# Performance work log

Measured on AMD Instinct MI355X. Metric: run time of the kernel, lower is better.

Reference implementation:

```python
import jax, jax.numpy as jnp
import numpy as np

NUM_HEADS = 16
NEG_INF = -1e9  # matches torch source's -1000000000.0 additive mask
ROPE_BASE = 10000.0


def _rope(t):
    """Rotary position embedding, half-rotation form. t: [B, H, S, D]."""
    D = t.shape[-1]
    S = t.shape[2]
    inv_freq = 1.0 / (ROPE_BASE ** (jnp.arange(0, D, 2, dtype=jnp.float32) / D))  # [D/2]
    pos = jnp.arange(S, dtype=jnp.float32)
    freqs = pos[:, None] * inv_freq[None, :]          # [S, D/2]
    cos = jnp.cos(freqs)[None, None]                  # [1,1,S,D/2]
    sin = jnp.sin(freqs)[None, None]
    t1, t2 = t[..., : D // 2], t[..., D // 2 :]
    return jnp.concatenate([t1 * cos - t2 * sin, t1 * sin + t2 * cos], axis=-1)


def setup_inputs() -> dict:
    key = jax.random.key(0)
    kx, kq, kk, kv, ko = jax.random.split(key, 5)
    B, S, Dm = 2, 2048, 1024
    w_scale = 0.02
    return {
        "x": jax.random.normal(kx, (B, S, Dm), dtype=jnp.float32),
        "attention_mask": jnp.ones((B, S), dtype=jnp.float32),
        "Wq": jax.random.normal(kq, (Dm, Dm), dtype=jnp.float32) * w_scale,
        "Wk": jax.random.normal(kk, (Dm, Dm), dtype=jnp.float32) * w_scale,
        "Wv": jax.random.normal(kv, (Dm, Dm), dtype=jnp.float32) * w_scale,
        "Wo": jax.random.normal(ko, (Dm, Dm), dtype=jnp.float32) * w_scale,
    }


def reference(x, attention_mask, Wq, Wk, Wv, Wo):
    B, S, Dm = x.shape
    H = NUM_HEADS
    Hd = Dm // H

    def to_heads(t):  # [B,S,Dm] -> [B,H,S,Hd]
        return t.reshape(B, S, H, Hd).transpose(0, 2, 1, 3)

    q = _rope(to_heads(x @ Wq))
    k = _rope(to_heads(x @ Wk))
    v = to_heads(x @ Wv)

    scaling = 1.0 / np.sqrt(Hd).astype(np.float32)
    scores = jnp.einsum("bhqd,bhkd->bhqk", q, k) * scaling  # [B,H,S,S]

    # causal additive mask (triu of -1e9 above diagonal), as in apply_masking
    causal = jnp.triu(jnp.full((S, S), NEG_INF, dtype=scores.dtype), k=1)
    # padding mask: (1 - mask) * -1e9 broadcast to [B,1,1,S]
    amask = (1.0 - attention_mask)[:, None, None, :] * NEG_INF
    scores = scores + causal[None, None] + amask

    weights = jax.nn.softmax(scores, axis=-1)
    out = jnp.einsum("bhqk,bhkd->bhqd", weights, v)  # [B,H,S,Hd]
    out = out.transpose(0, 2, 1, 3).reshape(B, S, Dm)
    return out @ Wo
```

## Files before the change

### kernel.cpp

```cpp
#include <hip/hip_runtime.h>

typedef unsigned short u16;
typedef unsigned int u32;
typedef __attribute__((ext_vector_type(8))) short short8;
typedef __attribute__((ext_vector_type(4))) short s4v;
typedef __attribute__((ext_vector_type(4))) float f32x4;

#define S_LEN 2048
#define NH 16
#define HD 64
#define DM 1024

#if __has_builtin(__builtin_amdgcn_mfma_f32_16x16x16_bf16)
#define MFMA_K16(a, b, c) __builtin_amdgcn_mfma_f32_16x16x16_bf16(a, b, c, 0, 0, 0)
#else
#define MFMA_K16(a, b, c) __builtin_amdgcn_mfma_f32_16x16x16bf16_1k(a, b, c, 0, 0, 0)
#endif

__device__ __forceinline__ u16 f2bf(float f) {
    union { float f; u32 u; } v; v.f = f;
    u32 u = v.u;
    u32 r = u + 0x7fffu + ((u >> 16) & 1u);
    return (u16)(r >> 16);
}
__device__ __forceinline__ float bf2f(u16 h) {
    union { u32 u; float f; } v; v.u = ((u32)h) << 16;
    return v.f;
}

__device__ __forceinline__ u32 cvtpk_bf16(float lo, float hi) {
    u32 r;
    asm("v_cvt_pk_bf16_f32 %0, %1, %2" : "=v"(r) : "v"(lo), "v"(hi));
    return r;
}

__device__ __forceinline__ void load_lds16(const u16* g, u16* l) {
    __builtin_amdgcn_global_load_lds((const __attribute__((address_space(1))) void*)g,
                                     (__attribute__((address_space(3))) void*)l, 16, 0, 0);
}

__global__ __launch_bounds__(256) void cvt_bf16(const float* __restrict__ in, u16* __restrict__ out, int n) {
    int i = (blockIdx.x * 256 + threadIdx.x) * 4;
    if (i < n) {
        float4 v = *(const float4*)(in + i);
        ushort4 o;
        o.x = f2bf(v.x); o.y = f2bf(v.y); o.z = f2bf(v.z); o.w = f2bf(v.w);
        *(ushort4*)(out + i) = o;
    }
}

__global__ __launch_bounds__(256) void transpose_w4(const float* __restrict__ W0, const float* __restrict__ W1,
                                                    const float* __restrict__ W2, const float* __restrict__ W3,
                                                    u16* __restrict__ T0, u16* __restrict__ T1,
                                                    u16* __restrict__ T2, u16* __restrict__ T3) {
    __shared__ float tile[32][33];
    int z = blockIdx.z;
    const float* W = (z == 0) ? W0 : (z == 1) ? W1 : (z == 2) ? W2 : W3;
    u16* Wt = (z == 0) ? T0 : (z == 1) ? T1 : (z == 2) ? T2 : T3;
    int tx = threadIdx.x, ty = threadIdx.y;
    int k0 = blockIdx.y * 32, n0 = blockIdx.x * 32;
    #pragma unroll
    for (int j = 0; j < 32; j += 8)
        tile[ty + j][tx] = W[(size_t)(k0 + ty + j) * DM + n0 + tx];
    __syncthreads();
    #pragma unroll
    for (int j = 0; j < 32; j += 8)
        Wt[(size_t)(n0 + ty + j) * DM + k0 + tx] = f2bf(tile[tx][ty + j]);
}

template<int MODE, int NI>
__global__ __launch_bounds__(256) void gemm128(const u16* __restrict__ A, const u16* __restrict__ Bt,
                                               u16* __restrict__ Qh, u16* __restrict__ Kh,
                                               u16* __restrict__ Vh, float* __restrict__ Cf) {
    __shared__ u16 Al[128 * 64];
    __shared__ u16 Bl[NI * 32 * 64];
    const int K = DM;
    int tid = threadIdx.x;
    int wave = tid >> 6, lane = tid & 63, g = lane >> 4, ln = lane & 15;
    int wm = (wave >> 1) * 64, wn = (wave & 1) * (NI * 16);
    size_t mb0 = (size_t)blockIdx.y * 128, nb0 = (size_t)blockIdx.x * (NI * 32);

    f32x4 acc[4][NI];
    #pragma unroll
    for (int i = 0; i < 4; i++)
        #pragma unroll
        for (int j = 0; j < NI; j++)
            acc[i][j] = (f32x4){0.f, 0.f, 0.f, 0.f};

    int srow = lane >> 3;
    int scol = (lane & 7) ^ srow;
    const u16* Ag = A + (mb0 + wave * 32 + srow) * K + scol * 8;
    u16* Alw = Al + wave * 2048;
    const u16* Bg;
    u16* Blw;
    if (NI == 4) {
        Bg = Bt + (nb0 + wave * 32 + srow) * K + scol * 8;
        Blw = Bl + wave * 2048;
    } else {
        Bg = Bt + (nb0 + wave * 16 + srow) * K + scol * 8;
        Blw = Bl + wave * 1024;
    }
    int cswz = ln & 7;

    #pragma unroll
    for (int c = 0; c < 4; c++)
        load_lds16(Ag + (size_t)(c * 8) * K, Alw + c * 512);
    #pragma unroll
    for (int c = 0; c < (NI == 4 ? 4 : 2); c++)
        load_lds16(Bg + (size_t)(c * 8) * K, Blw + c * 512);

    for (int k0 = 0; k0 < K; k0 += 64) {
        __syncthreads();

        short8 af[2][4], bf[2][NI];
        #pragma unroll
        for (int ks = 0; ks < 2; ks++) {
            #pragma unroll
            for (int i = 0; i < 4; i++)
                af[ks][i] = *(const short8*)&Al[(wm + i * 16 + ln) * 64 + (((ks * 4 + g) ^ cswz) * 8)];
            #pragma unroll
            for (int i = 0; i < NI; i++)
                bf[ks][i] = *(const short8*)&Bl[(wn + i * 16 + ln) * 64 + (((ks * 4 + g) ^ cswz) * 8)];
        }

        __syncthreads();

        if (k0 + 64 < K) {
            #pragma unroll
            for (int c = 0; c < 4; c++)
                load_lds16(Ag + (size_t)(c * 8) * K + k0 + 64, Alw + c * 512);
            #pragma unroll
            for (int c = 0; c < (NI == 4 ? 4 : 2); c++)
                load_lds16(Bg + (size_t)(c * 8) * K + k0 + 64, Blw + c * 512);
        }

        #pragma unroll
        for (int ks = 0; ks < 2; ks++)
            #pragma unroll
            for (int mi = 0; mi < 4; mi++)
                #pragma unroll
                for (int ni = 0; ni < NI; ni++)
                    acc[mi][ni] = __builtin_amdgcn_mfma_f32_16x16x32_bf16(af[ks][mi], bf[ks][ni], acc[mi][ni], 0, 0, 0);
    }

    if (MODE == 1) {
        #pragma unroll
        for (int mi = 0; mi < 4; mi++)
            #pragma unroll
            for (int ni = 0; ni < NI; ni++)
                #pragma unroll
                for (int r = 0; r < 4; r++) {
                    int m = (int)mb0 + wm + mi * 16 + g * 4 + r;
                    int n = (int)nb0 + wn + ni * 16 + ln;
                    Cf[(size_t)m * DM + n] = acc[mi][ni][r];
                }
    } else {
        int nbase = (int)nb0 + wn;
        int which = nbase >> 10;
        int h = (nbase & (DM - 1)) >> 6;
        if (which < 2) {
            u16* dst = (which == 0) ? Qh : Kh;
            float inv0 = exp2f(-0.4152408746976557f * (float)ln);
            float inv1 = exp2f(-0.4152408746976557f * (float)(16 + ln));
            #pragma unroll
            for (int mi = 0; mi < 4; mi++) {
                #pragma unroll
                for (int r = 0; r < 4; r++) {
                    int m = (int)mb0 + wm + mi * 16 + g * 4 + r;
                    int b = m >> 11, s = m & (S_LEN - 1);
                    float fs = (float)s;
                    float sn0, cs0, sn1, cs1;
                    __sincosf(fs * inv0, &sn0, &cs0);
                    __sincosf(fs * inv1, &sn1, &cs1);
                    float a0 = acc[mi][0][r], a1 = acc[mi][1][r];
                    float a2 = acc[mi][2][r], a3 = acc[mi][3][r];
                    size_t base = ((size_t)(b * NH + h) * S_LEN + s) * HD;
                    dst[base + ln]      = f2bf(a0 * cs0 - a2 * sn0);
                    dst[base + 16 + ln] = f2bf(a1 * cs1 - a3 * sn1);
                    dst[base + 32 + ln] = f2bf(a0 * sn0 + a2 * cs0);
                    dst[base + 48 + ln] = f2bf(a1 * sn1 + a3 * cs1);
                }
            }
        } else {
            #pragma unroll
            for (int mi = 0; mi < 4; mi++) {
                #pragma unroll
                for (int r = 0; r < 4; r++) {
                    int m = (int)mb0 + wm + mi * 16 + g * 4 + r;
                    int b = m >> 11, s = m & (S_LEN - 1);
                    size_t base = ((size_t)(b * NH + h) * S_LEN + s) * HD;
                    #pragma unroll
                    for (int ni = 0; ni < 4; ni++)
                        Vh[base + ni * 16 + ln] = f2bf(acc[mi][ni][r]);
                }
            }
        }
    }
}

__global__ __launch_bounds__(256) void vtrans(const u16* __restrict__ Vh, u16* __restrict__ Vt) {
    __shared__ u16 t[64][70];
    int tid = threadIdx.x;
    int s0 = blockIdx.x * 64, bh = blockIdx.y;
    int r = tid >> 2, c = (tid & 3) * 8;
    const u16* src = Vh + ((size_t)bh * S_LEN + s0) * HD;
    *(short8*)&t[r][c]      = *(const short8*)(src + (size_t)r * HD + c);
    *(short8*)&t[r][c + 32] = *(const short8*)(src + (size_t)r * HD + c + 32);
    __syncthreads();
    u16* dst = Vt + ((size_t)bh * HD + r) * S_LEN + s0;
    short8 o0, o1;
    #pragma unroll
    for (int j = 0; j < 8; j++) {
        o0[j] = (short)t[c + j][r];
        o1[j] = (short)t[c + 32 + j][r];
    }
    *(short8*)(dst + c)      = o0;
    *(short8*)(dst + c + 32) = o1;
}

__global__ __launch_bounds__(512, 4) void flash_kernel(const u16* __restrict__ Qh, const u16* __restrict__ Kh,
                                                       const u16* __restrict__ Vt, const float* __restrict__ amask,
                                                       u16* __restrict__ Op0, u16* __restrict__ Op1,
                                                       u16* __restrict__ Op2, u16* __restrict__ Op3,
                                                       float* __restrict__ L0, float* __restrict__ L1,
                                                       float* __restrict__ L2, float* __restrict__ L3) {
    __shared__ u16 Kl[2][64 * 64];
    __shared__ u16 Vl[2][64 * 64];
    __shared__ float Ml[2][64];
    int tid = threadIdx.x;
    int wave = tid >> 6, lane = tid & 63, g = lane >> 4, ln = lane & 15;
    int i = (int)blockIdx.x;
    int xcd = i & 7;
    int j = i >> 3;
    int bh = xcd * 4 + (j >> 6);
    int inner = j & 63;
    int qblk = 15 - (inner >> 2);
    int sp = inner & 3;
    int b = bh >> 4;
    int q0 = qblk * 128 + wave * 16;
    int qv = q0 + ln;
    const u16* Qb = Qh + (size_t)bh * (S_LEN * HD);
    const u16* Kb = Kh + (size_t)bh * (S_LEN * HD);
    const u16* Vb = Vt + (size_t)bh * (S_LEN * HD);
    const float* am = amask + b * S_LEN;

    short8 qa0 = *(const short8*)(Qb + (size_t)(q0 + ln) * HD + g * 8);
    short8 qa1 = *(const short8*)(Qb + (size_t)(q0 + ln) * HD + 32 + g * 8);

    f32x4 O[4];
    #pragma unroll
    for (int i2 = 0; i2 < 4; i2++) O[i2] = (f32x4){0.f, 0.f, 0.f, 0.f};
    f32x4 Osum = (f32x4){0.f, 0.f, 0.f, 0.f};
    const s4v ones = (s4v){(short)0x3F80, (short)0x3F80, (short)0x3F80, (short)0x3F80};
    const float SCL = 0.125f * 1.4426950408889634f;
    const float MSCL = -1.4426950408889634e9f;

    int T = 2 * qblk + 2;
    int srow = tid >> 3, scid = tid & 7, s7 = srow & 7;
    int stoff = srow * 64 + ((scid ^ s7) * 8);
    const u16* KgL = Kb + (size_t)srow * HD + ((scid ^ s7) * 8);
    const u16* VgP = Vb + (size_t)srow * S_LEN + scid * 8;
    bool vswap = (wave & 1);

    int l7 = ln & 7;
    int kc0 = (g ^ l7) * 8;
    int kc1 = ((4 + g) ^ l7) * 8;
    int rbq = ln * 64;
    int vcoff[4];
    #pragma unroll
    for (int n0 = 0; n0 < 4; n0++)
        vcoff[n0] = (((n0 * 2 + (g >> 1)) ^ l7) * 8) + ((((g & 1) ^ (ln >> 3)) & 1) * 4);

    load_lds16(KgL + (size_t)(sp * 64) * HD, &Kl[0][wave * 512]);
    short8 vR = *(const short8*)(VgP + sp * 64);
    float mR = 0.f;
    if (tid < 64) mR = (1.0f - am[sp * 64 + tid]) * MSCL;
    int cur = 0;

    for (int kt = sp; kt < T; kt += 4) {
        int kbase = kt * 64;
        short8 vS = vR;
        if (vswap) vS = __builtin_shufflevector(vR, vR, 4, 5, 6, 7, 0, 1, 2, 3);
        *(short8*)(Vl[cur] + stoff) = vS;
        if (tid < 64) Ml[cur][tid] = mR;
        __syncthreads();

        if (kt + 4 < T) {
            load_lds16(KgL + (size_t)(kbase + 256) * HD, &Kl[cur ^ 1][wave * 512]);
            vR = *(const short8*)(VgP + (kbase + 256));
            if (tid < 64) mR = (1.0f - am[kbase + 256 + tid]) * MSCL;
        }

        if (kbase <= q0 + 15) {
            const u16* Klc = Kl[cur];
            const u16* Vlc = Vl[cur];
            u32 pk[4][2];
            bool needmask = (kbase + 63 > q0);

            if (!needmask) {
                #pragma unroll
                for (int n0 = 0; n0 < 4; n0++) {
                    const u16* kr = Klc + (n0 * 16) * 64 + rbq;
                    short8 kb0 = *(const short8*)(kr + kc0);
                    short8 kb1 = *(const short8*)(kr + kc1);
                    f32x4 sv = (f32x4){0.f, 0.f, 0.f, 0.f};
                    sv = __builtin_amdgcn_mfma_f32_16x16x32_bf16(kb0, qa0, sv, 0, 0, 0);
                    sv = __builtin_amdgcn_mfma_f32_16x16x32_bf16(kb1, qa1, sv, 0, 0, 0);
                    f32x4 mkv = *(f32x4*)&Ml[cur][n0 * 16 + g * 4];
                    float p[4];
                    #pragma unroll
                    for (int r = 0; r < 4; r++)
                        p[r] = exp2f(sv[r] * SCL + mkv[r]);
                    pk[n0][0] = cvtpk_bf16(p[0], p[1]);
                    pk[n0][1] = cvtpk_bf16(p[2], p[3]);
                }
            } else {
                #pragma unroll
                for (int n0 = 0; n0 < 4; n0++) {
                    const u16* kr = Klc + (n0 * 16) * 64 + rbq;
                    short8 kb0 = *(const short8*)(kr + kc0);
                    short8 kb1 = *(const short8*)(kr + kc1);
                    f32x4 sv = (f32x4){0.f, 0.f, 0.f, 0.f};
                    sv = __builtin_amdgcn_mfma_f32_16x16x32_bf16(kb0, qa0, sv, 0, 0, 0);
                    sv = __builtin_amdgcn_mfma_f32_16x16x32_bf16(kb1, qa1, sv, 0, 0, 0);
                    f32x4 mkv = *(f32x4*)&Ml[cur][n0 * 16 + g * 4];
                    int keyb = kbase + n0 * 16 + g * 4;
                    float p[4];
                    #pragma unroll
                    for (int r = 0; r < 4; r++) {
                        float s2 = sv[r] * SCL + mkv[r];
                        if (keyb + r > qv) s2 = -1.0e9f;
                        p[r] = exp2f(s2);
                    }
                    pk[n0][0] = cvtpk_bf16(p[0], p[1]);
                    pk[n0][1] = cvtpk_bf16(p[2], p[3]);
                }
            }

            __builtin_amdgcn_s_setprio(1);
            #pragma unroll
            for (int n0 = 0; n0 < 4; n0++) {
                union { u32 u[2]; s4v v; } pb;
                pb.u[0] = pk[n0][0];
                pb.u[1] = pk[n0][1];
                Osum = MFMA_K16(ones, pb.v, Osum);
            }
            #pragma unroll
            for (int t = 0; t < 4; t++) {
                const u16* vr = Vlc + (t * 16) * 64 + rbq;
                #pragma unroll
                for (int n0 = 0; n0 < 4; n0++) {
                    s4v va = *(const s4v*)(vr + vcoff[n0]);
                    union { u32 u[2]; s4v v; } pb;
                    pb.u[0] = pk[n0][0];
                    pb.u[1] = pk[n0][1];
                    O[t] = MFMA_K16(va, pb.v, O[t]);
                }
            }
            __builtin_amdgcn_s_setprio(0);
        }
        cur ^= 1;
    }

    u16* Od = (sp == 0) ? Op0 : (sp == 1) ? Op1 : (sp == 2) ? Op2 : Op3;
    float* Ld = (sp == 0) ? L0 : (sp == 1) ? L1 : (sp == 2) ? L2 : L3;
    if (lane < 16) Ld[(size_t)bh * S_LEN + q0 + ln] = Osum[0];
    size_t obase = (size_t)bh * (HD * S_LEN) + q0 + ln;
    #pragma unroll
    for (int t = 0; t < 4; t++)
        #pragma unroll
        for (int r = 0; r < 4; r++)
            Od[obase + (size_t)(t * 16 + g * 4 + r) * S_LEN] = f2bf(O[t][r]);
}

__global__ __launch_bounds__(256) void flash_reduce(const u16* __restrict__ Op0, const u16* __restrict__ Op1,
                                                    const u16* __restrict__ Op2, const u16* __restrict__ Op3,
                                                    const float* __restrict__ L0, const float* __restrict__ L1,
                                                    const float* __restrict__ L2, const float* __restrict__ L3,
                                                    u16* __restrict__ attn) {
    __shared__ float t[64][65];
    int tid = threadIdx.x;
    int qt = blockIdx.x, bh = blockIdx.y;
    int b = bh >> 4, h = bh & (NH - 1);
    #pragma unroll
    for (int it = 0; it < 2; it++) {
        int idx = tid + it * 256;
        int d = idx >> 3, c = (idx & 7) * 8;
        size_t off = (size_t)bh * (HD * S_LEN) + (size_t)d * S_LEN + qt * 64 + c;
        short8 a0 = *(const short8*)(Op0 + off);
        short8 a1 = *(const short8*)(Op1 + off);
        short8 a2 = *(const short8*)(Op2 + off);
        short8 a3 = *(const short8*)(Op3 + off);
        #pragma unroll
        for (int j = 0; j < 8; j++)
            t[d][c + j] = bf2f((u16)a0[j]) + bf2f((u16)a1[j]) + bf2f((u16)a2[j]) + bf2f((u16)a3[j]);
    }
    __syncthreads();
    int qr = tid >> 2, dc = (tid & 3) * 16;
    int qg = qt * 64 + qr;
    size_t li = (size_t)bh * S_LEN + qg;
    float inv = 1.0f / (L0[li] + L1[li] + L2[li] + L3[li]);
    short8 o0, o1;
    #pragma unroll
    for (int j = 0; j < 8; j++) {
        o0[j] = (short)f2bf(t[dc + j][qr] * inv);
        o1[j] = (short)f2bf(t[dc + 8 + j][qr] * inv);
    }
    u16* dst = attn + ((size_t)b * S_LEN + qg) * DM + h * HD + dc;
    *(short8*)dst = o0;
    *(short8*)(dst + 8) = o1;
}

extern "C" void kernel_launch(void* const* d_in, const int* in_sizes, int n_in,
                              void* d_out, int out_size, void* d_ws, size_t ws_size,
                              hipStream_t stream) {
    const float* x     = (const float*)d_in[0];
    const float* amask = (const float*)d_in[1];
    const float* Wq    = (const float*)d_in[2];
    const float* Wk    = (const float*)d_in[3];
    const float* Wv    = (const float*)d_in[4];
    const float* Wo    = (const float*)d_in[5];
    float* out = (float*)d_out;
    char* ws = (char*)d_ws;

    u16* x_bf   = (u16*)(ws);
    u16* Op1    = (u16*)(ws);
    u16* Wqkv_t = (u16*)(ws + 8388608);
    float* L0   = (float*)(ws + 8388608);
    float* L1   = (float*)(ws + 8650752);
    float* L2   = (float*)(ws + 8912896);
    float* L3   = (float*)(ws + 9175040);
    u16* Wo_t   = (u16*)(ws + 14680064);
    u16* Qh     = (u16*)(ws + 16777216);
    u16* Kh     = (u16*)(ws + 25165824);
    u16* Vt     = (u16*)(ws + 33554432);
    u16* attnF  = (u16*)(ws + 33554432);
    u16* Vh     = (u16*)(ws + 41943040);
    u16* Op0    = (u16*)(ws + 41943040);
    u16* Op2    = (u16*)d_out;
    u16* Op3    = (u16*)d_out + 4194304;

    cvt_bf16<<<4096, 256, 0, stream>>>(x, x_bf, 2 * S_LEN * DM);

    transpose_w4<<<dim3(32, 32, 4), dim3(32, 8), 0, stream>>>(
        Wq, Wk, Wv, Wo, Wqkv_t, Wqkv_t + 1048576, Wqkv_t + 2097152, Wo_t);

    gemm128<0, 4><<<dim3(24, 32), 256, 0, stream>>>(x_bf, Wqkv_t, Qh, Kh, Vh, nullptr);

    vtrans<<<dim3(32, 2 * NH), 256, 0, stream>>>(Vh, Vt);

    flash_kernel<<<dim3(2048), 512, 0, stream>>>(Qh, Kh, Vt, amask,
                                                 Op0, Op1, Op2, Op3, L0, L1, L2, L3);

    flash_reduce<<<dim3(32, 2 * NH), 256, 0, stream>>>(Op0, Op1, Op2, Op3,
                                                       L0, L1, L2, L3, attnF);

    gemm128<1, 2><<<dim3(16, 32), 256, 0, stream>>>(attnF, Wo_t, nullptr, nullptr, nullptr, out);
}
```

Measured before the change: 189.7 us.

## Halve flash split-K factor to two and fuse prep conversion kernels

The x-to-bf16 conversion and the four weight transposes now run in one launch, which saves a kernel launch. The flash attention split over the key dimension drops from four partitions to two, so the grid shrinks to 1024 blocks and each block loops over twice as many key tiles. The reduce kernel reads only two partial outputs and two partial sums, which cuts memory traffic and removes the use of the output buffer as scratch. The cost is lower parallelism in the flash kernel and a longer serial loop per block, which could hurt occupancy or load balance under causal masking.

```diff
diff --git a/kernel.cpp b/kernel.cpp
--- a/kernel.cpp
+++ b/kernel.cpp
@@ -39,33 +39,36 @@
                                      (__attribute__((address_space(3))) void*)l, 16, 0, 0);
 }
 
-__global__ __launch_bounds__(256) void cvt_bf16(const float* __restrict__ in, u16* __restrict__ out, int n) {
-    int i = (blockIdx.x * 256 + threadIdx.x) * 4;
-    if (i < n) {
-        float4 v = *(const float4*)(in + i);
+__global__ __launch_bounds__(256) void prep_fused(const float* __restrict__ x, u16* __restrict__ x_bf,
+                                                  const float* __restrict__ W0, const float* __restrict__ W1,
+                                                  const float* __restrict__ W2, const float* __restrict__ W3,
+                                                  u16* __restrict__ T0, u16* __restrict__ T1,
+                                                  u16* __restrict__ T2, u16* __restrict__ T3) {
+    __shared__ float tile[32][33];
+    int bid = blockIdx.x;
+    int tid = threadIdx.x;
+    if (bid < 4096) {
+        int i = (bid * 256 + tid) * 4;
+        float4 v = *(const float4*)(x + i);
         ushort4 o;
         o.x = f2bf(v.x); o.y = f2bf(v.y); o.z = f2bf(v.z); o.w = f2bf(v.w);
-        *(ushort4*)(out + i) = o;
-    }
-}
-
-__global__ __launch_bounds__(256) void transpose_w4(const float* __restrict__ W0, const float* __restrict__ W1,
-                                                    const float* __restrict__ W2, const float* __restrict__ W3,
-                                                    u16* __restrict__ T0, u16* __restrict__ T1,
-                                                    u16* __restrict__ T2, u16* __restrict__ T3) {
-    __shared__ float tile[32][33];
-    int z = blockIdx.z;
-    const float* W = (z == 0) ? W0 : (z == 1) ? W1 : (z == 2) ? W2 : W3;
-    u16* Wt = (z == 0) ? T0 : (z == 1) ? T1 : (z == 2) ? T2 : T3;
-    int tx = threadIdx.x, ty = threadIdx.y;
-    int k0 = blockIdx.y * 32, n0 = blockIdx.x * 32;
-    #pragma unroll
-    for (int j = 0; j < 32; j += 8)
-        tile[ty + j][tx] = W[(size_t)(k0 + ty + j) * DM + n0 + tx];
-    __syncthreads();
-    #pragma unroll
-    for (int j = 0; j < 32; j += 8)
-        Wt[(size_t)(n0 + ty + j) * DM + k0 + tx] = f2bf(tile[tx][ty + j]);
+        *(ushort4*)(x_bf + i) = o;
+    } else {
+        int wid = bid - 4096;
+        int z = wid >> 10;
+        const float* W = (z == 0) ? W0 : (z == 1) ? W1 : (z == 2) ? W2 : W3;
+        u16* Wt = (z == 0) ? T0 : (z == 1) ? T1 : (z == 2) ? T2 : T3;
+        int rem = wid & 1023;
+        int n0 = (rem & 31) * 32, k0 = (rem >> 5) * 32;
+        int tx = tid & 31, ty = tid >> 5;
+        #pragma unroll
+        for (int j = 0; j < 32; j += 8)
+            tile[ty + j][tx] = W[(size_t)(k0 + ty + j) * DM + n0 + tx];
+        __syncthreads();
+        #pragma unroll
+        for (int j = 0; j < 32; j += 8)
+            Wt[(size_t)(n0 + ty + j) * DM + k0 + tx] = f2bf(tile[tx][ty + j]);
+    }
 }
 
 template<int MODE, int NI>
@@ -221,9 +224,7 @@
 __global__ __launch_bounds__(512, 4) void flash_kernel(const u16* __restrict__ Qh, const u16* __restrict__ Kh,
                                                        const u16* __restrict__ Vt, const float* __restrict__ amask,
                                                        u16* __restrict__ Op0, u16* __restrict__ Op1,
-                                                       u16* __restrict__ Op2, u16* __restrict__ Op3,
-                                                       float* __restrict__ L0, float* __restrict__ L1,
-                                                       float* __restrict__ L2, float* __restrict__ L3) {
+                                                       float* __restrict__ L0, float* __restrict__ L1) {
     __shared__ u16 Kl[2][64 * 64];
     __shared__ u16 Vl[2][64 * 64];
     __shared__ float Ml[2][64];
@@ -232,10 +233,10 @@
     int i = (int)blockIdx.x;
     int xcd = i & 7;
     int j = i >> 3;
-    int bh = xcd * 4 + (j >> 6);
-    int inner = j & 63;
-    int qblk = 15 - (inner >> 2);
-    int sp = inner & 3;
+    int bh = xcd * 4 + (j >> 5);
+    int inner = j & 31;
+    int qblk = 15 - (inner >> 1);
+    int sp = inner & 1;
     int b = bh >> 4;
     int q0 = qblk * 128 + wave * 16;
     int qv = q0 + ln;
@@ -277,7 +278,7 @@
     if (tid < 64) mR = (1.0f - am[sp * 64 + tid]) * MSCL;
     int cur = 0;
 
-    for (int kt = sp; kt < T; kt += 4) {
+    for (int kt = sp; kt < T; kt += 2) {
         int kbase = kt * 64;
         short8 vS = vR;
         if (vswap) vS = __builtin_shufflevector(vR, vR, 4, 5, 6, 7, 0, 1, 2, 3);
@@ -285,10 +286,10 @@
         if (tid < 64) Ml[cur][tid] = mR;
         __syncthreads();
 
-        if (kt + 4 < T) {
-            load_lds16(KgL + (size_t)(kbase + 256) * HD, &Kl[cur ^ 1][wave * 512]);
-            vR = *(const short8*)(VgP + (kbase + 256));
-            if (tid < 64) mR = (1.0f - am[kbase + 256 + tid]) * MSCL;
+        if (kt + 2 < T) {
+            load_lds16(KgL + (size_t)(kbase + 128) * HD, &Kl[cur ^ 1][wave * 512]);
+            vR = *(const short8*)(VgP + (kbase + 128));
+            if (tid < 64) mR = (1.0f - am[kbase + 128 + tid]) * MSCL;
         }
 
         if (kbase <= q0 + 15) {
@@ -362,8 +363,8 @@
         cur ^= 1;
     }
 
-    u16* Od = (sp == 0) ? Op0 : (sp == 1) ? Op1 : (sp == 2) ? Op2 : Op3;
-    float* Ld = (sp == 0) ? L0 : (sp == 1) ? L1 : (sp == 2) ? L2 : L3;
+    u16* Od = sp ? Op1 : Op0;
+    float* Ld = sp ? L1 : L0;
     if (lane < 16) Ld[(size_t)bh * S_LEN + q0 + ln] = Osum[0];
     size_t obase = (size_t)bh * (HD * S_LEN) + q0 + ln;
     #pragma unroll
@@ -374,9 +375,7 @@
 }
 
 __global__ __launch_bounds__(256) void flash_reduce(const u16* __restrict__ Op0, const u16* __restrict__ Op1,
-                                                    const u16* __restrict__ Op2, const u16* __restrict__ Op3,
                                                     const float* __restrict__ L0, const float* __restrict__ L1,
-                                                    const float* __restrict__ L2, const float* __restrict__ L3,
                                                     u16* __restrict__ attn) {
     __shared__ float t[64][65];
     int tid = threadIdx.x;
@@ -389,17 +388,15 @@
         size_t off = (size_t)bh * (HD * S_LEN) + (size_t)d * S_LEN + qt * 64 + c;
         short8 a0 = *(const short8*)(Op0 + off);
         short8 a1 = *(const short8*)(Op1 + off);
-        short8 a2 = *(const short8*)(Op2 + off);
-        short8 a3 = *(const short8*)(Op3 + off);
         #pragma unroll
         for (int j = 0; j < 8; j++)
-            t[d][c + j] = bf2f((u16)a0[j]) + bf2f((u16)a1[j]) + bf2f((u16)a2[j]) + bf2f((u16)a3[j]);
+            t[d][c + j] = bf2f((u16)a0[j]) + bf2f((u16)a1[j]);
     }
     __syncthreads();
     int qr = tid >> 2, dc = (tid & 3) * 16;
     int qg = qt * 64 + qr;
     size_t li = (size_t)bh * S_LEN + qg;
-    float inv = 1.0f / (L0[li] + L1[li] + L2[li] + L3[li]);
+    float inv = 1.0f / (L0[li] + L1[li]);
     short8 o0, o1;
     #pragma unroll
     for (int j = 0; j < 8; j++) {
@@ -428,8 +425,6 @@
     u16* Wqkv_t = (u16*)(ws + 8388608);
     float* L0   = (float*)(ws + 8388608);
     float* L1   = (float*)(ws + 8650752);
-    float* L2   = (float*)(ws + 8912896);
-    float* L3   = (float*)(ws + 9175040);
     u16* Wo_t   = (u16*)(ws + 14680064);
     u16* Qh     = (u16*)(ws + 16777216);
     u16* Kh     = (u16*)(ws + 25165824);
@@ -437,23 +432,17 @@
     u16* attnF  = (u16*)(ws + 33554432);
     u16* Vh     = (u16*)(ws + 41943040);
     u16* Op0    = (u16*)(ws + 41943040);
-    u16* Op2    = (u16*)d_out;
-    u16* Op3    = (u16*)d_out + 4194304;
-
-    cvt_bf16<<<4096, 256, 0, stream>>>(x, x_bf, 2 * S_LEN * DM);
-
-    transpose_w4<<<dim3(32, 32, 4), dim3(32, 8), 0, stream>>>(
-        Wq, Wk, Wv, Wo, Wqkv_t, Wqkv_t + 1048576, Wqkv_t + 2097152, Wo_t);
+
+    prep_fused<<<8192, 256, 0, stream>>>(x, x_bf, Wq, Wk, Wv, Wo,
+                                         Wqkv_t, Wqkv_t + 1048576, Wqkv_t + 2097152, Wo_t);
 
     gemm128<0, 4><<<dim3(24, 32), 256, 0, stream>>>(x_bf, Wqkv_t, Qh, Kh, Vh, nullptr);
 
     vtrans<<<dim3(32, 2 * NH), 256, 0, stream>>>(Vh, Vt);
 
-    flash_kernel<<<dim3(2048), 512, 0, stream>>>(Qh, Kh, Vt, amask,
-                                                 Op0, Op1, Op2, Op3, L0, L1, L2, L3);
-
-    flash_reduce<<<dim3(32, 2 * NH), 256, 0, stream>>>(Op0, Op1, Op2, Op3,
-                                                       L0, L1, L2, L3, attnF);
+    flash_kernel<<<dim3(1024), 512, 0, stream>>>(Qh, Kh, Vt, amask, Op0, Op1, L0, L1);
+
+    flash_reduce<<<dim3(32, 2 * NH), 256, 0, stream>>>(Op0, Op1, L0, L1, attnF);
 
     gemm128<1, 2><<<dim3(16, 32), 256, 0, stream>>>(attnF, Wo_t, nullptr, nullptr, nullptr, out);
 }
```

Result: no change. 191.9 us (+1.2%).
